# Performance work log

Measured on AMD Instinct MI355X. Metric: run time of the kernel, lower is better.

Reference implementation:

```python
import jax, jax.numpy as jnp
import numpy as np

B, S, K, N = 2, 4096, 4096, 4096
BLOCKSIZE = 128  # GPTQ group size


def _unpack_rows(q):
    # int32 [K//8, N] -> int32 [K, N], 8 nibbles packed along dim 0 (little-endian)
    shifts = (jnp.arange(8, dtype=jnp.int32) * 4)
    nib = (q[:, None, :] >> shifts[None, :, None]) & 0xF  # [K//8, 8, N]
    return nib.reshape(q.shape[0] * 8, q.shape[1])


def _unpack_cols(q):
    # int32 [G, N//8] -> int32 [G, N], 8 nibbles packed along dim 1
    shifts = (jnp.arange(8, dtype=jnp.int32) * 4)
    nib = (q[:, :, None] >> shifts[None, None, :]) & 0xF  # [G, N//8, 8]
    return nib.reshape(q.shape[0], q.shape[1] * 8)


def _dequant(qweight, scales, qzeros, blocksize):
    # GPTQ int4 dequant: w[k, n] = (q[k, n] - z[g, n]) * s[g, n], g = k // blocksize
    w_int = _unpack_rows(qweight).astype(jnp.float32)          # [K, N]
    zeros = _unpack_cols(qzeros).astype(jnp.float32)           # [G, N]
    z = jnp.repeat(zeros, blocksize, axis=0)                   # [K, N]
    s = jnp.repeat(scales, blocksize, axis=0)                  # [K, N]
    return (w_int - z) * s


def setup_inputs() -> dict:
    key = jax.random.key(0)
    ks = jax.random.split(key, 6)
    inp = jax.random.normal(ks[0], (B, S, K), dtype=jnp.float32)
    residual = jax.random.normal(ks[1], (B, S, N), dtype=jnp.float32)
    qweight = jax.random.randint(ks[2], (K // 8, N), 0, 2147483647, dtype=jnp.int32)
    qzeros = jax.random.randint(ks[3], (K // BLOCKSIZE, N // 8), 0, 2147483647, dtype=jnp.int32)
    scales = jax.random.uniform(ks[4], (K // BLOCKSIZE, N), dtype=jnp.float32, minval=1e-3, maxval=1e-2)
    bias = jax.random.normal(ks[5], (N,), dtype=jnp.float32)
    return {"input": inp, "residual": residual, "qweight": qweight,
            "scales": scales, "qzeros": qzeros, "bias": bias}


def reference(input, residual, qweight, scales, qzeros, bias):
    # Fused: dequant(int4 GPTQ) -> GEMM -> +bias -> +residual (mm_bias_add_int4)
    w = _dequant(qweight, scales, qzeros, BLOCKSIZE)           # [K, N]
    out = jnp.einsum('bsk,kn->bsn', input, w) + bias + residual
    return out
```

## Files before the change

kernel.cpp:

```cpp
#include <hip/hip_runtime.h>
#include <hip/hip_bf16.h>
#include <stdint.h>

using bf16 = __hip_bfloat16;
typedef __attribute__((ext_vector_type(8))) short short8;
typedef __attribute__((ext_vector_type(4))) float floatx4;

#define DEVINL __device__ __forceinline__

constexpr int K_DIM = 4096;
constexpr int N_DIM = 4096;
constexpr int M_DIM = 8192;

constexpr int BM = 128, BN = 128, BK = 32;
constexpr int NBLK_N = N_DIM / BN;

DEVINL void gload_lds16(const void* g, void* l) {
  __builtin_amdgcn_global_load_lds((const __attribute__((address_space(1))) void*)g,
                                   (__attribute__((address_space(3))) void*)l,
                                   16, 0, 0);
}

__global__ __launch_bounds__(256) void k_a_convert(const float* __restrict__ a,
                                                   bf16* __restrict__ o) {
  int t = blockIdx.x * 256 + threadIdx.x;
  const float4* a4 = (const float4*)a;
  float4 v0 = a4[2 * t], v1 = a4[2 * t + 1];
  bf16 h[8];
  h[0] = __float2bfloat16(v0.x); h[1] = __float2bfloat16(v0.y);
  h[2] = __float2bfloat16(v0.z); h[3] = __float2bfloat16(v0.w);
  h[4] = __float2bfloat16(v1.x); h[5] = __float2bfloat16(v1.y);
  h[6] = __float2bfloat16(v1.z); h[7] = __float2bfloat16(v1.w);
  ((uint4*)o)[t] = *(const uint4*)h;
}

__global__ __launch_bounds__(256) void k_dequant(const int* __restrict__ qw,
                                                 const float* __restrict__ scales,
                                                 const int* __restrict__ qz,
                                                 bf16* __restrict__ wt) {
  int t = blockIdx.x * 256 + threadIdx.x;
  int kp = t & (K_DIM / 8 - 1);
  int n  = t >> 9;
  int q = qw[kp * N_DIM + n];
  int g = kp >> 4;
  float s = scales[g * N_DIM + n];
  int zword = qz[g * (N_DIM / 8) + (n >> 3)];
  float z = (float)((zword >> ((n & 7) * 4)) & 0xF);
  float nzs = -z * s;
  bf16 h[8];
#pragma unroll
  for (int i = 0; i < 8; ++i) {
    float w = fmaf((float)((q >> (4 * i)) & 0xF), s, nzs);
    h[i] = __float2bfloat16(w);
  }
  ((uint4*)wt)[n * (K_DIM / 8) + kp] = *(const uint4*)h;
}

template <bool A_IS_BF16>
__global__ __launch_bounds__(256, 2) void k_gemm(const void* __restrict__ a_ptr,
                                                 const bf16* __restrict__ wt,
                                                 const float* __restrict__ bias,
                                                 const float* __restrict__ residual,
                                                 float* __restrict__ out) {
  __shared__ __align__(16) bf16 As[BM * BK];
  __shared__ __align__(16) bf16 Bs[BN * BK];

  const int tid  = threadIdx.x;
  const int lane = tid & 63;
  const int wave = tid >> 6;
  const int wr = wave >> 1, wc = wave & 1;
  const int quad = lane >> 4, lq = lane & 15;

  const int bid = blockIdx.x;
  const int bm = bid / NBLK_N, bn = bid % NBLK_N;
  const int m0 = bm * BM, n0 = bn * BN;

  floatx4 acc[4][4] = {};

  const int st_row = lane >> 2;
  const int st_c8  = (lane & 3) * 8;

  const bf16*  a_bf = (const bf16*)a_ptr;
  const float* a_f  = (const float*)a_ptr;

  for (int k0 = 0; k0 < K_DIM; k0 += BK) {
    __syncthreads();
#pragma unroll
    for (int j = 0; j < 2; ++j) {
      int q = wave + j * 4;
      const bf16* g = wt + (size_t)(n0 + q * 16 + st_row) * K_DIM + k0 + st_c8;
      gload_lds16(g, &Bs[q * 512]);
    }
    if (A_IS_BF16) {
#pragma unroll
      for (int j = 0; j < 2; ++j) {
        int q = wave + j * 4;
        const bf16* g = a_bf + (size_t)(m0 + q * 16 + st_row) * K_DIM + k0 + st_c8;
        gload_lds16(g, &As[q * 512]);
      }
    } else {
      int row = tid >> 1, cb = (tid & 1) * 16;
      const float* srcf = a_f + (size_t)(m0 + row) * K_DIM + k0 + cb;
      float4 v0 = ((const float4*)srcf)[0];
      float4 v1 = ((const float4*)srcf)[1];
      float4 v2 = ((const float4*)srcf)[2];
      float4 v3 = ((const float4*)srcf)[3];
      bf16 h[16];
      h[0]  = __float2bfloat16(v0.x); h[1]  = __float2bfloat16(v0.y);
      h[2]  = __float2bfloat16(v0.z); h[3]  = __float2bfloat16(v0.w);
      h[4]  = __float2bfloat16(v1.x); h[5]  = __float2bfloat16(v1.y);
      h[6]  = __float2bfloat16(v1.z); h[7]  = __float2bfloat16(v1.w);
      h[8]  = __float2bfloat16(v2.x); h[9]  = __float2bfloat16(v2.y);
      h[10] = __float2bfloat16(v2.z); h[11] = __float2bfloat16(v2.w);
      h[12] = __float2bfloat16(v3.x); h[13] = __float2bfloat16(v3.y);
      h[14] = __float2bfloat16(v3.z); h[15] = __float2bfloat16(v3.w);
      *(uint4*)&As[row * BK + cb]     = *(const uint4*)h;
      *(uint4*)&As[row * BK + cb + 8] = *(const uint4*)(h + 8);
    }
    __syncthreads();

    short8 afr[4], bfr[4];
#pragma unroll
    for (int mi = 0; mi < 4; ++mi)
      afr[mi] = *(const short8*)&As[(wr * 64 + mi * 16 + lq) * BK + quad * 8];
#pragma unroll
    for (int ni = 0; ni < 4; ++ni)
      bfr[ni] = *(const short8*)&Bs[(wc * 64 + ni * 16 + lq) * BK + quad * 8];
#pragma unroll
    for (int mi = 0; mi < 4; ++mi)
#pragma unroll
      for (int ni = 0; ni < 4; ++ni)
        acc[mi][ni] = __builtin_amdgcn_mfma_f32_16x16x32_bf16(afr[mi], bfr[ni],
                                                              acc[mi][ni], 0, 0, 0);
  }

#pragma unroll
  for (int ni = 0; ni < 4; ++ni) {
    int col = n0 + wc * 64 + ni * 16 + lq;
    float bv = bias[col];
#pragma unroll
    for (int mi = 0; mi < 4; ++mi) {
      int rbase = m0 + wr * 64 + mi * 16 + quad * 4;
#pragma unroll
      for (int r = 0; r < 4; ++r) {
        size_t idx = (size_t)(rbase + r) * N_DIM + col;
        out[idx] = acc[mi][ni][r] + bv + residual[idx];
      }
    }
  }
}

extern "C" void kernel_launch(void* const* d_in, const int* in_sizes, int n_in,
                              void* d_out, int out_size, void* d_ws, size_t ws_size,
                              hipStream_t stream) {
  const float* input    = (const float*)d_in[0];
  const float* residual = (const float*)d_in[1];
  const int*   qweight  = (const int*)d_in[2];
  const float* scales   = (const float*)d_in[3];
  const int*   qzeros   = (const int*)d_in[4];
  const float* bias     = (const float*)d_in[5];
  float* out = (float*)d_out;

  const size_t wt_bytes = (size_t)N_DIM * K_DIM * sizeof(bf16);
  const size_t a_bytes  = (size_t)M_DIM * K_DIM * sizeof(bf16);

  bf16* wt = (bf16*)d_ws;
  k_dequant<<<(N_DIM * (K_DIM / 8)) / 256, 256, 0, stream>>>(qweight, scales, qzeros, wt);

  if (ws_size >= wt_bytes + a_bytes) {
    bf16* a_bf = (bf16*)((char*)d_ws + wt_bytes);
    k_a_convert<<<(M_DIM * K_DIM / 8) / 256, 256, 0, stream>>>(input, a_bf);
    k_gemm<true><<<(M_DIM / BM) * (N_DIM / BN), 256, 0, stream>>>(a_bf, wt, bias, residual, out);
  } else {
    k_gemm<false><<<(M_DIM / BM) * (N_DIM / BN), 256, 0, stream>>>(input, wt, bias, residual, out);
  }
}
```

Before: 664.4 us.

## Swizzle GEMM LDS tiles and transpose dequant output through shared memory

```diff
diff --git a/kernel.cpp b/kernel.cpp
--- a/kernel.cpp
+++ b/kernel.cpp
@@ -38,11 +38,16 @@
                                                  const float* __restrict__ scales,
                                                  const int* __restrict__ qz,
                                                  bf16* __restrict__ wt) {
-  int t = blockIdx.x * 256 + threadIdx.x;
-  int kp = t & (K_DIM / 8 - 1);
-  int n  = t >> 9;
+  __shared__ __align__(16) uint4 lds[32 * 8];
+  const int b = blockIdx.x;
+  const int kp0 = (b & 63) * 8;
+  const int n0  = (b >> 6) * 32;
+  const int t = threadIdx.x;
+  const int n_l = t & 31, kp_l = t >> 5;
+  const int n = n0 + n_l, kp = kp0 + kp_l;
+
   int q = qw[kp * N_DIM + n];
-  int g = kp >> 4;
+  int g = kp0 >> 4;
   float s = scales[g * N_DIM + n];
   int zword = qz[g * (N_DIM / 8) + (n >> 3)];
   float z = (float)((zword >> ((n & 7) * 4)) & 0xF);
@@ -53,7 +58,11 @@
     float w = fmaf((float)((q >> (4 * i)) & 0xF), s, nzs);
     h[i] = __float2bfloat16(w);
   }
-  ((uint4*)wt)[n * (K_DIM / 8) + kp] = *(const uint4*)h;
+  lds[n_l * 8 + (kp_l ^ (n_l & 7))] = *(const uint4*)h;
+  __syncthreads();
+  const int n_o = t >> 3, kp_o = t & 7;
+  uint4 v = lds[n_o * 8 + (kp_o ^ (n_o & 7))];
+  ((uint4*)wt)[(size_t)(n0 + n_o) * (K_DIM / 8) + kp0 + kp_o] = v;
 }
 
 template <bool A_IS_BF16>
@@ -70,6 +79,8 @@
   const int wave = tid >> 6;
   const int wr = wave >> 1, wc = wave & 1;
   const int quad = lane >> 4, lq = lane & 15;
+  const int sw = (lane >> 1) & 3;
+  const int rd_c8 = (quad ^ sw) * 8;
 
   const int bid = blockIdx.x;
   const int bm = bid / NBLK_N, bn = bid % NBLK_N;
@@ -78,7 +89,7 @@
   floatx4 acc[4][4] = {};
 
   const int st_row = lane >> 2;
-  const int st_c8  = (lane & 3) * 8;
+  const int st_c8  = ((lane & 3) ^ ((lane >> 3) & 3)) * 8;
 
   const bf16*  a_bf = (const bf16*)a_ptr;
   const float* a_f  = (const float*)a_ptr;
@@ -99,8 +110,9 @@
         gload_lds16(g, &As[q * 512]);
       }
     } else {
-      int row = tid >> 1, cb = (tid & 1) * 16;
-      const float* srcf = a_f + (size_t)(m0 + row) * K_DIM + k0 + cb;
+      int row = tid >> 1, c0 = (tid & 1) * 2;
+      int rsw = (row >> 1) & 3;
+      const float* srcf = a_f + (size_t)(m0 + row) * K_DIM + k0 + c0 * 8;
       float4 v0 = ((const float4*)srcf)[0];
       float4 v1 = ((const float4*)srcf)[1];
       float4 v2 = ((const float4*)srcf)[2];
@@ -114,18 +126,18 @@
       h[10] = __float2bfloat16(v2.z); h[11] = __float2bfloat16(v2.w);
       h[12] = __float2bfloat16(v3.x); h[13] = __float2bfloat16(v3.y);
       h[14] = __float2bfloat16(v3.z); h[15] = __float2bfloat16(v3.w);
-      *(uint4*)&As[row * BK + cb]     = *(const uint4*)h;
-      *(uint4*)&As[row * BK + cb + 8] = *(const uint4*)(h + 8);
+      *(uint4*)&As[row * BK + ((c0 ^ rsw) * 8)]       = *(const uint4*)h;
+      *(uint4*)&As[row * BK + (((c0 + 1) ^ rsw) * 8)] = *(const uint4*)(h + 8);
     }
     __syncthreads();
 
     short8 afr[4], bfr[4];
 #pragma unroll
     for (int mi = 0; mi < 4; ++mi)
-      afr[mi] = *(const short8*)&As[(wr * 64 + mi * 16 + lq) * BK + quad * 8];
+      afr[mi] = *(const short8*)&As[(wr * 64 + mi * 16 + lq) * BK + rd_c8];
 #pragma unroll
     for (int ni = 0; ni < 4; ++ni)
-      bfr[ni] = *(const short8*)&Bs[(wc * 64 + ni * 16 + lq) * BK + quad * 8];
+      bfr[ni] = *(const short8*)&Bs[(wc * 64 + ni * 16 + lq) * BK + rd_c8];
 #pragma unroll
     for (int mi = 0; mi < 4; ++mi)
 #pragma unroll
@@ -165,7 +177,7 @@
   const size_t a_bytes  = (size_t)M_DIM * K_DIM * sizeof(bf16);
 
   bf16* wt = (bf16*)d_ws;
-  k_dequant<<<(N_DIM * (K_DIM / 8)) / 256, 256, 0, stream>>>(qweight, scales, qzeros, wt);
+  k_dequant<<<64 * 128, 256, 0, stream>>>(qweight, scales, qzeros, wt);
 
   if (ws_size >= wt_bytes + a_bytes) {
     bf16* a_bf = (bf16*)((char*)d_ws + wt_bytes);
```

New measurement: 648.6 us. 1.02x faster.
